# Kernel optimization log

Measured on AMD Instinct MI355X. Metric: run time of the kernel, lower is better.

## Reference

```python
import jax, jax.numpy as jnp
import numpy as np

B, G, A = 8, 32768, 64          # molecules, grid points/molecule, atomic orbitals/molecule
N_ORB, DIM, L_FUNC, N_OUT = 400, 128, 3, 1
EPS = 1e-12


def setup_inputs() -> dict:
    key = jax.random.key(0)
    ks = jax.random.split(key, 12)
    # interatomic/grid distances in Bohr-ish range (strictly positive)
    distance_matrices = jax.random.uniform(ks[0], (B, G, A), jnp.float32) * 10.0 + 0.05
    quantum_numbers = jax.random.randint(ks[1], (B, A), 0, 3, jnp.int32)   # q-1 in {0,1,2}
    atomic_orbitals = jax.random.randint(ks[2], (B, A), 0, N_ORB, jnp.int32)
    N_electrons = jax.random.uniform(ks[3], (B,), jnp.float32) * 50.0 + 10.0
    coef_table = jax.random.normal(ks[4], (N_ORB, DIM), jnp.float32) * 0.1
    zeta_table = jnp.ones((N_ORB, 1), jnp.float32)   # nn.init.ones_
    W_pre_w = jax.random.normal(ks[5], (DIM, 1), jnp.float32) * 0.1
    W_pre_b = jax.random.normal(ks[6], (DIM,), jnp.float32) * 0.01
    W_func_w = jax.random.normal(ks[7], (L_FUNC, DIM, DIM), jnp.float32) * (1.0 / np.sqrt(DIM))
    W_func_b = jax.random.normal(ks[8], (L_FUNC, DIM), jnp.float32) * 0.01
    W_prop_w = jax.random.normal(ks[9], (N_OUT, DIM), jnp.float32) * (1.0 / np.sqrt(DIM))
    W_prop_b = jax.random.normal(ks[10], (N_OUT,), jnp.float32) * 0.01
    return dict(distance_matrices=distance_matrices, quantum_numbers=quantum_numbers,
                atomic_orbitals=atomic_orbitals, N_electrons=N_electrons,
                coef_table=coef_table, zeta_table=zeta_table,
                W_pre_w=W_pre_w, W_pre_b=W_pre_b,
                W_func_w=W_func_w, W_func_b=W_func_b,
                W_prop_w=W_prop_w, W_prop_b=W_prop_b)


def reference(distance_matrices, quantum_numbers, atomic_orbitals, N_electrons,
              coef_table, zeta_table, W_pre_w, W_pre_b, W_func_w, W_func_b,
              W_prop_w, W_prop_b):
    d = distance_matrices                                   # [B,G,A]
    q = quantum_numbers.astype(jnp.float32) + 1.0           # principal quantum number {1,2,3}
    z = zeta_table[atomic_orbitals][..., 0]                 # [B,A] orbital exponents
    # GTO basis: d^(q-1) * exp(-(z*d)^2); block-diagonal padding (d=1e6 -> 0) is
    # equivalent to this batched per-molecule form.
    gto = d ** (q[:, None, :] - 1.0) * jnp.exp(-(z[:, None, :] * d) ** 2)
    gto = gto / jnp.maximum(jnp.sqrt(jnp.sum(gto * gto, 1, keepdims=True)), EPS)
    # per-molecule L2-normalized LCAO coefficients (F.normalize over AO axis)
    c = coef_table[atomic_orbitals]                         # [B,A,D]
    c = c / jnp.maximum(jnp.sqrt(jnp.sum(c * c, 1, keepdims=True)), EPS)
    # LCAO: molecular orbitals, then per-molecule normalization over grid points
    mo = jnp.einsum('bga,bad->bgd', gto, c)                 # [B,G,D]
    mo = mo / jnp.maximum(jnp.sqrt(jnp.sum(mo * mo, 1, keepdims=True)), EPS)
    mo = jnp.sqrt(N_electrons / DIM)[:, None, None] * mo
    densities = jnp.sum(mo * mo, -1, keepdims=True)         # [B,G,1]
    # DNN-based energy functional
    v = densities * W_pre_w[:, 0] + W_pre_b                 # [B,G,D]  (Linear(1,dim))
    for l in range(L_FUNC):
        v = jax.nn.relu(jnp.einsum('bgd,ed->bge', v, W_func_w[l]) + W_func_b[l])
    final = jnp.sum(v, 1)                                   # operation == 'sum' over grid
    E_xcH = final @ W_prop_w.T + W_prop_b                   # [B,N_OUT]
    return E_xcH
```

## Files before the change

kernel.cpp:

```cpp
#include <hip/hip_runtime.h>
#include <stdint.h>


#define BB 8
#define GG 32768
#define AA 64
#define DD 128
#define EPSF 1e-12f

#define WS_M    0u
#define WS_ZQ   131072u
#define WS_CN   135168u
#define WS_UW   397312u
#define WS_CCT  398336u
#define WS_W2   529408u
#define WS_W3   562176u

typedef __attribute__((ext_vector_type(8))) short bf16x8;
typedef __attribute__((ext_vector_type(4))) float f32x4;

__device__ __forceinline__ unsigned short f2bf(float f) {
    union { float f; unsigned int u; } x; x.f = f;
    unsigned int u = x.u + 0x7FFFu + ((x.u >> 16) & 1u);
    return (unsigned short)(u >> 16);
}
__device__ __forceinline__ float bfround(float f) {
    union { float f; unsigned int u; } x; x.f = f;
    unsigned int u = x.u + 0x7FFFu + ((x.u >> 16) & 1u);
    x.u = u & 0xFFFF0000u;
    return x.f;
}

__global__ __launch_bounds__(256)
void k_prep(const int* __restrict__ q, const int* __restrict__ ao,
            const float* __restrict__ coef, const float* __restrict__ zeta,
            const float* __restrict__ wpre_w, const float* __restrict__ wpre_b,
            const float* __restrict__ wfunc_w, const float* __restrict__ wfunc_b,
            const float* __restrict__ wprop_b, float* __restrict__ out,
            char* __restrict__ ws)
{
    int tid = blockIdx.x * 256 + threadIdx.x;
    if (tid < 32768) {
        int lsel = tid >> 14;
        int idx = tid & 16383;
        unsigned short* dst = (unsigned short*)(ws + (lsel == 0 ? WS_W2 : WS_W3));
        dst[idx] = f2bf(wfunc_w[(lsel + 1) * 16384 + idx]);
    } else if (tid < 33792) {
        int i = tid - 32768;
        int b = i >> 7, dd = i & 127;
        float s = 0.f;
        for (int a = 0; a < AA; ++a) {
            float v = coef[ao[b * AA + a] * DD + dd];
            s += v * v;
        }
        float inv = 1.f / fmaxf(sqrtf(s), EPSF);
        float* cn = (float*)(ws + WS_CN);
        for (int a = 0; a < AA; ++a)
            cn[((size_t)b * AA + a) * DD + dd] = coef[ao[b * AA + a] * DD + dd] * inv;
    } else if (tid < 34304) {
        int i = tid - 33792;
        int b = i >> 6, a = i & 63;
        float* zq = (float*)(ws + WS_ZQ);
        zq[(b * AA + a) * 2 + 0] = zeta[ao[b * AA + a]];
        zq[(b * AA + a) * 2 + 1] = (float)q[b * AA + a];
    } else if (tid < 34432) {
        int e = tid - 34304;
        float su = 0.f, sw = 0.f;
        for (int dd = 0; dd < DD; ++dd) {
            float wv = wfunc_w[e * DD + dd];
            su += wv * wpre_w[dd];
            sw += wv * wpre_b[dd];
        }
        float* uw = (float*)(ws + WS_UW);
        uw[e] = su;
        uw[128 + e] = sw + wfunc_b[e];
    } else if (tid < 34440) {
        out[tid - 34432] = wprop_b[0];
    } else if (tid < 67208) {
        ((float*)(ws + WS_M))[tid - 34440] = 0.f;
    }
}

__global__ __launch_bounds__(128)
void k_corr(const float* __restrict__ wfunc_w, const float* __restrict__ wfunc_b,
            const float* __restrict__ wprop_w, float* __restrict__ out,
            char* __restrict__ ws)
{
    __shared__ float v1e[128], v1b[128], v2e[128], v2b[128];
    __shared__ float part[2];
    int t = threadIdx.x;
    const float* uw = (const float*)(ws + WS_UW);
    float w0 = uw[128 + t];
    float r = fmaxf(w0, 0.f);
    v1e[t] = r;
    v1b[t] = bfround(r);
    __syncthreads();
    float ze = wfunc_b[128 + t], zb = ze;
    for (int dd = 0; dd < 128; ++dd) {
        float wv = wfunc_w[16384 + t * 128 + dd];
        ze += wv * v1e[dd];
        zb += bfround(wv) * v1b[dd];
    }
    v2e[t] = fmaxf(ze, 0.f);
    v2b[t] = bfround(fmaxf(zb, 0.f));
    __syncthreads();
    float ye = wfunc_b[256 + t], yb = ye;
    for (int dd = 0; dd < 128; ++dd) {
        float wv = wfunc_w[32768 + t * 128 + dd];
        ye += wv * v2e[dd];
        yb += bfround(wv) * v2b[dd];
    }
    float wpv = wprop_w[t];
    float diff = (fmaxf(ye, 0.f) - fmaxf(yb, 0.f)) * wpv;
    #pragma unroll
    for (int m = 1; m < 64; m <<= 1) diff += __shfl_xor(diff, m);
    if ((t & 63) == 0) part[t >> 6] = diff;
    __syncthreads();
    if (t == 0) {
        float corr = (part[0] + part[1]) * (float)GG;
        #pragma unroll
        for (int b = 0; b < BB; ++b) atomicAdd(&out[b], corr);
    }
}

__global__ __launch_bounds__(512, 4)
void k_M(const float* __restrict__ dmat, char* __restrict__ ws)
{
    __shared__ unsigned short gs[8192];
    const int b = blockIdx.y;
    const int chunk = blockIdx.x;
    const int t = threadIdx.x;
    const int g4 = t & 31;
    const int a4 = t >> 5;

    const float* zqp = (const float*)(ws + WS_ZQ) + b * 128;
    float4 zq0 = *(const float4*)(zqp + a4 * 8);
    float4 zq1 = *(const float4*)(zqp + a4 * 8 + 4);
    float zz[4] = {zq0.x, zq0.z, zq1.x, zq1.z};
    float qm[4] = {zq0.y, zq0.w, zq1.y, zq1.w};

    const int wv = t >> 6, l = t & 63;
    const int ta = wv >> 1, tb0 = (wv & 1) * 2;
    const int lrow = l & 15, lk = l >> 4;

    const float* dbase = dmat + (size_t)b * GG * AA + (size_t)chunk * 512 * AA;

    f32x4 acc[2];
    acc[0] = (f32x4){0.f, 0.f, 0.f, 0.f};
    acc[1] = (f32x4){0.f, 0.f, 0.f, 0.f};

    float4 pf[4];
    #pragma unroll
    for (int gg = 0; gg < 4; ++gg)
        pf[gg] = *(const float4*)(dbase + (size_t)(g4 * 4 + gg) * AA + a4 * 4);

    for (int tt = 0; tt < 4; ++tt) {
        float gv[4][4];
        #pragma unroll
        for (int gg = 0; gg < 4; ++gg) {
            float dvv[4] = {pf[gg].x, pf[gg].y, pf[gg].z, pf[gg].w};
            #pragma unroll
            for (int j = 0; j < 4; ++j) {
                float ttv = zz[j] * dvv[j];
                float ex = __expf(-ttv * ttv);
                float pw = (qm[j] < 0.5f) ? 1.f : ((qm[j] < 1.5f) ? dvv[j] : dvv[j] * dvv[j]);
                gv[gg][j] = pw * ex;
            }
        }
        if (tt < 3) {
            #pragma unroll
            for (int gg = 0; gg < 4; ++gg)
                pf[gg] = *(const float4*)(dbase + (size_t)((tt + 1) * 128 + g4 * 4 + gg) * AA + a4 * 4);
        }
        #pragma unroll
        for (int j = 0; j < 4; ++j) {
            int a = a4 * 4 + j;
            unsigned int lo = (unsigned int)f2bf(gv[0][j]) | ((unsigned int)f2bf(gv[1][j]) << 16);
            unsigned int hi = (unsigned int)f2bf(gv[2][j]) | ((unsigned int)f2bf(gv[3][j]) << 16);
            int off = a * 256 + ((g4 * 8) ^ ((a & 7) << 4));
            *(uint2*)((char*)gs + off) = make_uint2(lo, hi);
        }
        __syncthreads();
        #pragma unroll
        for (int kt = 0; kt < 4; ++kt) {
            int colB = kt * 64 + lk * 16;
            int ra = ta * 16 + lrow;
            bf16x8 af = *(const bf16x8*)((const char*)gs + ra * 256 + (colB ^ ((ra & 7) << 4)));
            #pragma unroll
            for (int jj = 0; jj < 2; ++jj) {
                int rb = (tb0 + jj) * 16 + lrow;
                bf16x8 bv = *(const bf16x8*)((const char*)gs + rb * 256 + (colB ^ ((rb & 7) << 4)));
                acc[jj] = __builtin_amdgcn_mfma_f32_16x16x32_bf16(af, bv, acc[jj], 0, 0, 0);
            }
        }
        __syncthreads();
    }
    float* Mg = (float*)(ws + WS_M) + b * 4096;
    #pragma unroll
    for (int jj = 0; jj < 2; ++jj)
        #pragma unroll
        for (int r = 0; r < 4; ++r)
            atomicAdd(&Mg[(ta * 16 + lk * 4 + r) * 64 + (tb0 + jj) * 16 + lrow], acc[jj][r]);
}

__global__ __launch_bounds__(256)
void k_cct(const float* __restrict__ Ne, char* __restrict__ ws)
{
    __shared__ float M[64][64];
    __shared__ float e_s[128][65];
    __shared__ float inv_na[64];
    __shared__ float alpha[128];
    const int b = blockIdx.x, t = threadIdx.x;
    const float* Mg = (const float*)(ws + WS_M) + b * 4096;
    for (int i = t; i < 4096; i += 256) ((float*)M)[i] = Mg[i];
    __syncthreads();
    if (t < 64) inv_na[t] = 1.f / fmaxf(sqrtf(M[t][t]), EPSF);
    __syncthreads();
    const float* cn = (const float*)(ws + WS_CN) + (size_t)b * AA * DD;
    for (int i = t; i < 8192; i += 256) {
        int a = i >> 7, dd = i & 127;
        e_s[dd][a] = cn[a * DD + dd] * inv_na[a];
    }
    __syncthreads();
    const int d = t >> 1, half = t & 1;
    float y[32];
    #pragma unroll
    for (int j = 0; j < 32; ++j) y[j] = 0.f;
    for (int a = 0; a < 64; ++a) {
        float ea = e_s[d][a];
        const float4* Mr = (const float4*)&M[a][half * 32];
        #pragma unroll 8
        for (int j4 = 0; j4 < 8; ++j4) {
            float4 mv = Mr[j4];
            y[4 * j4 + 0] += ea * mv.x; y[4 * j4 + 1] += ea * mv.y;
            y[4 * j4 + 2] += ea * mv.z; y[4 * j4 + 3] += ea * mv.w;
        }
    }
    float s = 0.f;
    #pragma unroll 8
    for (int j = 0; j < 32; ++j) s += e_s[d][half * 32 + j] * y[j];
    s += __shfl_xor(s, 1);
    if (half == 0) alpha[d] = sqrtf(Ne[b] * (1.f / 128.f)) / fmaxf(sqrtf(s), EPSF);
    __syncthreads();
    unsigned short* cct = (unsigned short*)(ws + WS_CCT) + (size_t)b * 8192;
    for (int i = t; i < 8192; i += 256) {
        int dd = i >> 6, a = i & 63;
        cct[i] = f2bf(e_s[dd][a] * alpha[dd]);
    }
}

__global__ __launch_bounds__(512, 4)
void k_main(const float* __restrict__ dmat, const float* __restrict__ wfunc_b,
            const float* __restrict__ wprop_w, float* __restrict__ out,
            char* __restrict__ ws)
{
    __shared__ char bufA[32768];
    __shared__ float dens[128];
    __shared__ float bsum;

    const int t = threadIdx.x;
    const int b = blockIdx.x >> 8;
    const int tile = blockIdx.x & 255;

    const int wv = t >> 6, l = t & 63;
    const int gsel = wv >> 1, dsel = wv & 1;
    const int lrow = l & 15, lk = l >> 4;
    const int srow = t >> 2, q4 = t & 3;

    const char* Wcct = (const char*)(ws + WS_CCT) + (size_t)b * 16384u;
    const char* W2g  = (const char*)(ws + WS_W2);
    const char* W3g  = (const char*)(ws + WS_W3);
    const float* zqp = (const float*)(ws + WS_ZQ) + b * 128;
    const float* uwp = (const float*)(ws + WS_UW);

    if (t < 128) dens[t] = 0.f;
    if (t == 0) bsum = 0.f;

    {
        const float* drow = dmat + ((size_t)b * GG + (size_t)tile * 128 + srow) * AA + q4 * 16;
        #pragma unroll
        for (int c = 0; c < 2; ++c) {
            float4 d0 = *(const float4*)(drow + c * 8);
            float4 d1 = *(const float4*)(drow + c * 8 + 4);
            const float* zb = zqp + (q4 * 16 + c * 8) * 2;
            float dvv[8] = {d0.x, d0.y, d0.z, d0.w, d1.x, d1.y, d1.z, d1.w};
            unsigned int wd[4];
            #pragma unroll
            for (int h = 0; h < 4; ++h) {
                unsigned short q2[2];
                #pragma unroll
                for (int jj = 0; jj < 2; ++jj) {
                    int j = h * 2 + jj;
                    float zzv = zb[j * 2], qmv = zb[j * 2 + 1];
                    float dv = dvv[j];
                    float ttv = zzv * dv;
                    float ex = __expf(-ttv * ttv);
                    float pw = (qmv < 0.5f) ? 1.f : ((qmv < 1.5f) ? dv : dv * dv);
                    q2[jj] = f2bf(pw * ex);
                }
                wd[h] = (unsigned int)q2[0] | ((unsigned int)q2[1] << 16);
            }
            int colB = q4 * 32 + c * 16;
            *(uint4*)(bufA + srow * 128 + (colB ^ ((srow & 7) << 4))) =
                make_uint4(wd[0], wd[1], wd[2], wd[3]);
        }
    }
    __syncthreads();

    {
        f32x4 acc[2][4];
        #pragma unroll
        for (int i = 0; i < 2; ++i)
            #pragma unroll
            for (int j = 0; j < 4; ++j) acc[i][j] = (f32x4){0.f, 0.f, 0.f, 0.f};
        #pragma unroll
        for (int kt = 0; kt < 2; ++kt) {
            int colB = kt * 64 + lk * 16;
            bf16x8 af[2], bv[4];
            #pragma unroll
            for (int i = 0; i < 2; ++i) {
                int gr = (gsel * 2 + i) * 16 + lrow;
                af[i] = *(const bf16x8*)(bufA + gr * 128 + (colB ^ ((gr & 7) << 4)));
            }
            #pragma unroll
            for (int j = 0; j < 4; ++j) {
                int dr = (dsel * 4 + j) * 16 + lrow;
                bv[j] = *(const bf16x8*)(Wcct + dr * 128 + colB);
            }
            #pragma unroll
            for (int i = 0; i < 2; ++i)
                #pragma unroll
                for (int j = 0; j < 4; ++j)
                    acc[i][j] = __builtin_amdgcn_mfma_f32_16x16x32_bf16(af[i], bv[j], acc[i][j], 0, 0, 0);
        }
        #pragma unroll
        for (int i = 0; i < 2; ++i) {
            float ds4[4] = {0.f, 0.f, 0.f, 0.f};
            #pragma unroll
            for (int j = 0; j < 4; ++j)
                #pragma unroll
                for (int r = 0; r < 4; ++r) { float m = acc[i][j][r]; ds4[r] += m * m; }
            #pragma unroll
            for (int r = 0; r < 4; ++r) {
                float vv = ds4[r];
                vv += __shfl_xor(vv, 1); vv += __shfl_xor(vv, 2);
                vv += __shfl_xor(vv, 4); vv += __shfl_xor(vv, 8);
                if (lrow == 0) atomicAdd(&dens[(gsel * 2 + i) * 16 + lk * 4 + r], vv);
            }
        }
    }
    __syncthreads();

    {
        float dv = dens[srow];
        #pragma unroll
        for (int c = 0; c < 4; ++c) {
            int di0 = q4 * 32 + c * 8;
            float4 ua = *(const float4*)(uwp + di0);
            float4 ub = *(const float4*)(uwp + di0 + 4);
            float4 wa = *(const float4*)(uwp + 128 + di0);
            float4 wb = *(const float4*)(uwp + 128 + di0 + 4);
            float uu[8] = {ua.x, ua.y, ua.z, ua.w, ub.x, ub.y, ub.z, ub.w};
            float wwv[8] = {wa.x, wa.y, wa.z, wa.w, wb.x, wb.y, wb.z, wb.w};
            unsigned int wd[4];
            #pragma unroll
            for (int h = 0; h < 4; ++h) {
                unsigned short q2[2];
                #pragma unroll
                for (int jj = 0; jj < 2; ++jj)
                    q2[jj] = f2bf(fmaxf(dv * uu[h * 2 + jj] + wwv[h * 2 + jj], 0.f));
                wd[h] = (unsigned int)q2[0] | ((unsigned int)q2[1] << 16);
            }
            int colB = q4 * 64 + c * 16;
            *(uint4*)(bufA + srow * 256 + (colB ^ ((srow & 7) << 4))) =
                make_uint4(wd[0], wd[1], wd[2], wd[3]);
        }
    }
    __syncthreads();

    f32x4 acc2[2][4];
    {
        #pragma unroll
        for (int i = 0; i < 2; ++i)
            #pragma unroll
            for (int j = 0; j < 4; ++j) acc2[i][j] = (f32x4){0.f, 0.f, 0.f, 0.f};
        #pragma unroll
        for (int kt = 0; kt < 4; ++kt) {
            int colB = kt * 64 + lk * 16;
            bf16x8 af[2], bv[4];
            #pragma unroll
            for (int i = 0; i < 2; ++i) {
                int gr = (gsel * 2 + i) * 16 + lrow;
                af[i] = *(const bf16x8*)(bufA + gr * 256 + (colB ^ ((gr & 7) << 4)));
            }
            #pragma unroll
            for (int j = 0; j < 4; ++j) {
                int er = (dsel * 4 + j) * 16 + lrow;
                bv[j] = *(const bf16x8*)(W2g + er * 256 + colB);
            }
            #pragma unroll
            for (int i = 0; i < 2; ++i)
                #pragma unroll
                for (int j = 0; j < 4; ++j)
                    acc2[i][j] = __builtin_amdgcn_mfma_f32_16x16x32_bf16(af[i], bv[j], acc2[i][j], 0, 0, 0);
        }
    }
    __syncthreads();

    #pragma unroll
    for (int j = 0; j < 4; ++j) {
        int e = (dsel * 4 + j) * 16 + lrow;
        float bias = wfunc_b[128 + e];
        #pragma unroll
        for (int i = 0; i < 2; ++i)
            #pragma unroll
            for (int r = 0; r < 4; ++r) {
                int g = (gsel * 2 + i) * 16 + lk * 4 + r;
                float vv = fmaxf(acc2[i][j][r] + bias, 0.f);
                *(unsigned short*)(bufA + g * 256 + ((e * 2) ^ ((g & 7) << 4))) = f2bf(vv);
            }
    }
    __syncthreads();

    f32x4 acc3[2][4];
    {
        #pragma unroll
        for (int i = 0; i < 2; ++i)
            #pragma unroll
            for (int j = 0; j < 4; ++j) acc3[i][j] = (f32x4){0.f, 0.f, 0.f, 0.f};
        #pragma unroll
        for (int kt = 0; kt < 4; ++kt) {
            int colB = kt * 64 + lk * 16;
            bf16x8 af[2], bv[4];
            #pragma unroll
            for (int i = 0; i < 2; ++i) {
                int gr = (gsel * 2 + i) * 16 + lrow;
                af[i] = *(const bf16x8*)(bufA + gr * 256 + (colB ^ ((gr & 7) << 4)));
            }
            #pragma unroll
            for (int j = 0; j < 4; ++j) {
                int er = (dsel * 4 + j) * 16 + lrow;
                bv[j] = *(const bf16x8*)(W3g + er * 256 + colB);
            }
            #pragma unroll
            for (int i = 0; i < 2; ++i)
                #pragma unroll
                for (int j = 0; j < 4; ++j)
                    acc3[i][j] = __builtin_amdgcn_mfma_f32_16x16x32_bf16(af[i], bv[j], acc3[i][j], 0, 0, 0);
        }
    }

    float esum = 0.f;
    #pragma unroll
    for (int j = 0; j < 4; ++j) {
        int e = (dsel * 4 + j) * 16 + lrow;
        float bias = wfunc_b[256 + e], wpv = wprop_w[e];
        #pragma unroll
        for (int i = 0; i < 2; ++i)
            #pragma unroll
            for (int r = 0; r < 4; ++r)
                esum += fmaxf(acc3[i][j][r] + bias, 0.f) * wpv;
    }
    #pragma unroll
    for (int m = 1; m < 64; m <<= 1) esum += __shfl_xor(esum, m);
    if (l == 0) atomicAdd(&bsum, esum);
    __syncthreads();
    if (t == 0) atomicAdd(&out[b], bsum);
}

extern "C" void kernel_launch(void* const* d_in, const int* in_sizes, int n_in,
                              void* d_out, int out_size, void* d_ws, size_t ws_size,
                              hipStream_t stream)
{
    const float* dmat    = (const float*)d_in[0];
    const int*   q       = (const int*)d_in[1];
    const int*   ao      = (const int*)d_in[2];
    const float* Ne      = (const float*)d_in[3];
    const float* coef    = (const float*)d_in[4];
    const float* zeta    = (const float*)d_in[5];
    const float* wpre_w  = (const float*)d_in[6];
    const float* wpre_b  = (const float*)d_in[7];
    const float* wfunc_w = (const float*)d_in[8];
    const float* wfunc_b = (const float*)d_in[9];
    const float* wprop_w = (const float*)d_in[10];
    const float* wprop_b = (const float*)d_in[11];
    float* out = (float*)d_out;
    char*  ws  = (char*)d_ws;

    k_prep<<<263, 256, 0, stream>>>(q, ao, coef, zeta, wpre_w, wpre_b,
                                    wfunc_w, wfunc_b, wprop_b, out, ws);
    k_corr<<<1, 128, 0, stream>>>(wfunc_w, wfunc_b, wprop_w, out, ws);
    k_M<<<dim3(64, 8), 512, 0, stream>>>(dmat, ws);
    k_cct<<<8, 256, 0, stream>>>(Ne, ws);
    k_main<<<2048, 512, 0, stream>>>(dmat, wfunc_b, wprop_w, out, ws);
}
```

Baseline: 278.3 us.

## Restructure k_main to per-wave tiles in registers and replicate k_M atomics

k_main now assigns each wave its own 16 grid rows. The GTO values go straight into MFMA A-fragments from registers, and densities are reduced with shuffles instead of through shared memory. Most LDS staging and block barriers between the three GEMM stages go away, and blocks shrink to 256 threads. k_M is reorganized around 256-point chunks with double-buffered LDS and wider swizzles. Its atomic accumulation is spread over 8 replica buffers plus a reduction kernel to cut atomic contention, at the cost of an extra memset and an extra launch.

Measured after the change: 321.3 us. 1.15x slower.

```diff
diff --git a/kernel.cpp b/kernel.cpp
--- a/kernel.cpp
+++ b/kernel.cpp
@@ -15,6 +15,7 @@
 #define WS_CCT  398336u
 #define WS_W2   529408u
 #define WS_W3   562176u
+#define WS_M8   594944u
 
 typedef __attribute__((ext_vector_type(8))) short bf16x8;
 typedef __attribute__((ext_vector_type(4))) float f32x4;
@@ -29,6 +30,12 @@
     unsigned int u = x.u + 0x7FFFu + ((x.u >> 16) & 1u);
     x.u = u & 0xFFFF0000u;
     return x.f;
+}
+__device__ __forceinline__ float gto_eval(float dv, float zz, float qm) {
+    float ttv = zz * dv;
+    float ex = __expf(-ttv * ttv);
+    float pw = (qm < 0.5f) ? 1.f : ((qm < 1.5f) ? dv : dv * dv);
+    return pw * ex;
 }
 
 __global__ __launch_bounds__(256)
@@ -61,8 +68,8 @@
         int i = tid - 33792;
         int b = i >> 6, a = i & 63;
         float* zq = (float*)(ws + WS_ZQ);
-        zq[(b * AA + a) * 2 + 0] = zeta[ao[b * AA + a]];
-        zq[(b * AA + a) * 2 + 1] = (float)q[b * AA + a];
+        zq[b * 128 + a]      = zeta[ao[b * AA + a]];
+        zq[b * 128 + 64 + a] = (float)q[b * AA + a];
     } else if (tid < 34432) {
         int e = tid - 34304;
         float su = 0.f, sw = 0.f;
@@ -123,84 +130,86 @@
     }
 }
 
-__global__ __launch_bounds__(512, 4)
+template<int NREP>
+__global__ __launch_bounds__(256, 4)
 void k_M(const float* __restrict__ dmat, char* __restrict__ ws)
 {
-    __shared__ unsigned short gs[8192];
+    __shared__ unsigned short gs[2][8192];
     const int b = blockIdx.y;
     const int chunk = blockIdx.x;
     const int t = threadIdx.x;
-    const int g4 = t & 31;
-    const int a4 = t >> 5;
-
-    const float* zqp = (const float*)(ws + WS_ZQ) + b * 128;
-    float4 zq0 = *(const float4*)(zqp + a4 * 8);
-    float4 zq1 = *(const float4*)(zqp + a4 * 8 + 4);
-    float zz[4] = {zq0.x, zq0.z, zq1.x, zq1.z};
-    float qm[4] = {zq0.y, zq0.w, zq1.y, zq1.w};
-
+    const int g4 = t & 31, a8 = t >> 5;
     const int wv = t >> 6, l = t & 63;
-    const int ta = wv >> 1, tb0 = (wv & 1) * 2;
     const int lrow = l & 15, lk = l >> 4;
 
-    const float* dbase = dmat + (size_t)b * GG * AA + (size_t)chunk * 512 * AA;
-
-    f32x4 acc[2];
-    acc[0] = (f32x4){0.f, 0.f, 0.f, 0.f};
-    acc[1] = (f32x4){0.f, 0.f, 0.f, 0.f};
-
-    float4 pf[4];
-    #pragma unroll
-    for (int gg = 0; gg < 4; ++gg)
-        pf[gg] = *(const float4*)(dbase + (size_t)(g4 * 4 + gg) * AA + a4 * 4);
-
-    for (int tt = 0; tt < 4; ++tt) {
-        float gv[4][4];
+    const float* zzp = (const float*)(ws + WS_ZQ) + b * 128;
+    float4 za = *(const float4*)(zzp + a8 * 8);
+    float4 zbv = *(const float4*)(zzp + a8 * 8 + 4);
+    float4 qa = *(const float4*)(zzp + 64 + a8 * 8);
+    float4 qb = *(const float4*)(zzp + 64 + a8 * 8 + 4);
+    float zz8[8] = {za.x, za.y, za.z, za.w, zbv.x, zbv.y, zbv.z, zbv.w};
+    float qm8[8] = {qa.x, qa.y, qa.z, qa.w, qb.x, qb.y, qb.z, qb.w};
+
+    const float* dbase = dmat + ((size_t)b * GG + (size_t)chunk * 256) * AA;
+
+    #pragma unroll
+    for (int tt = 0; tt < 2; ++tt) {
+        float gv[4][8];
         #pragma unroll
         for (int gg = 0; gg < 4; ++gg) {
-            float dvv[4] = {pf[gg].x, pf[gg].y, pf[gg].z, pf[gg].w};
+            const float* rp = dbase + (size_t)(tt * 128 + g4 * 4 + gg) * AA + a8 * 8;
+            float4 x0 = *(const float4*)rp;
+            float4 x1 = *(const float4*)(rp + 4);
+            float dv8[8] = {x0.x, x0.y, x0.z, x0.w, x1.x, x1.y, x1.z, x1.w};
             #pragma unroll
-            for (int j = 0; j < 4; ++j) {
-                float ttv = zz[j] * dvv[j];
-                float ex = __expf(-ttv * ttv);
-                float pw = (qm[j] < 0.5f) ? 1.f : ((qm[j] < 1.5f) ? dvv[j] : dvv[j] * dvv[j]);
-                gv[gg][j] = pw * ex;
-            }
-        }
-        if (tt < 3) {
-            #pragma unroll
-            for (int gg = 0; gg < 4; ++gg)
-                pf[gg] = *(const float4*)(dbase + (size_t)((tt + 1) * 128 + g4 * 4 + gg) * AA + a4 * 4);
-        }
-        #pragma unroll
-        for (int j = 0; j < 4; ++j) {
-            int a = a4 * 4 + j;
+            for (int j = 0; j < 8; ++j) gv[gg][j] = gto_eval(dv8[j], zz8[j], qm8[j]);
+        }
+        #pragma unroll
+        for (int j = 0; j < 8; ++j) {
+            int a = a8 * 8 + j;
             unsigned int lo = (unsigned int)f2bf(gv[0][j]) | ((unsigned int)f2bf(gv[1][j]) << 16);
             unsigned int hi = (unsigned int)f2bf(gv[2][j]) | ((unsigned int)f2bf(gv[3][j]) << 16);
-            int off = a * 256 + ((g4 * 8) ^ ((a & 7) << 4));
-            *(uint2*)((char*)gs + off) = make_uint2(lo, hi);
-        }
-        __syncthreads();
+            *(uint2*)((char*)gs[tt] + a * 256 + ((g4 * 8) ^ ((a & 15) << 4))) = make_uint2(lo, hi);
+        }
+    }
+    __syncthreads();
+
+    f32x4 acc[4];
+    #pragma unroll
+    for (int rb = 0; rb < 4; ++rb) acc[rb] = (f32x4){0.f, 0.f, 0.f, 0.f};
+    #pragma unroll
+    for (int tt = 0; tt < 2; ++tt)
         #pragma unroll
         for (int kt = 0; kt < 4; ++kt) {
             int colB = kt * 64 + lk * 16;
-            int ra = ta * 16 + lrow;
-            bf16x8 af = *(const bf16x8*)((const char*)gs + ra * 256 + (colB ^ ((ra & 7) << 4)));
+            int ra = wv * 16 + lrow;
+            bf16x8 af = *(const bf16x8*)((const char*)gs[tt] + ra * 256 + (colB ^ ((ra & 15) << 4)));
             #pragma unroll
-            for (int jj = 0; jj < 2; ++jj) {
-                int rb = (tb0 + jj) * 16 + lrow;
-                bf16x8 bv = *(const bf16x8*)((const char*)gs + rb * 256 + (colB ^ ((rb & 7) << 4)));
-                acc[jj] = __builtin_amdgcn_mfma_f32_16x16x32_bf16(af, bv, acc[jj], 0, 0, 0);
+            for (int rb = 0; rb < 4; ++rb) {
+                int rr = rb * 16 + lrow;
+                bf16x8 bv = *(const bf16x8*)((const char*)gs[tt] + rr * 256 + (colB ^ ((rr & 15) << 4)));
+                acc[rb] = __builtin_amdgcn_mfma_f32_16x16x32_bf16(af, bv, acc[rb], 0, 0, 0);
             }
         }
-        __syncthreads();
-    }
-    float* Mg = (float*)(ws + WS_M) + b * 4096;
-    #pragma unroll
-    for (int jj = 0; jj < 2; ++jj)
+
+    float* Mg = (float*)(ws + (NREP > 1 ? WS_M8 + (unsigned)(chunk & (NREP - 1)) * 131072u
+                                        : WS_M)) + b * 4096;
+    #pragma unroll
+    for (int rb = 0; rb < 4; ++rb)
         #pragma unroll
         for (int r = 0; r < 4; ++r)
-            atomicAdd(&Mg[(ta * 16 + lk * 4 + r) * 64 + (tb0 + jj) * 16 + lrow], acc[jj][r]);
+            atomicAdd(&Mg[(wv * 16 + lk * 4 + r) * 64 + rb * 16 + lrow], acc[rb][r]);
+}
+
+__global__ __launch_bounds__(256)
+void k_red(char* __restrict__ ws)
+{
+    int i = blockIdx.x * 256 + threadIdx.x;
+    const float* rp = (const float*)(ws + WS_M8);
+    float s = 0.f;
+    #pragma unroll
+    for (int r = 0; r < 8; ++r) s += rp[r * 32768 + i];
+    ((float*)(ws + WS_M))[i] = s;
 }
 
 __global__ __launch_bounds__(256)
@@ -249,220 +258,139 @@
     }
 }
 
-__global__ __launch_bounds__(512, 4)
+__global__ __launch_bounds__(256, 4)
 void k_main(const float* __restrict__ dmat, const float* __restrict__ wfunc_b,
             const float* __restrict__ wprop_w, float* __restrict__ out,
             char* __restrict__ ws)
 {
-    __shared__ char bufA[32768];
-    __shared__ float dens[128];
+    __shared__ char v2buf[16384];
     __shared__ float bsum;
 
     const int t = threadIdx.x;
-    const int b = blockIdx.x >> 8;
-    const int tile = blockIdx.x & 255;
-
+    const int b = blockIdx.x >> 9;
+    const int tile = blockIdx.x & 511;
     const int wv = t >> 6, l = t & 63;
-    const int gsel = wv >> 1, dsel = wv & 1;
     const int lrow = l & 15, lk = l >> 4;
-    const int srow = t >> 2, q4 = t & 3;
-
-    const char* Wcct = (const char*)(ws + WS_CCT) + (size_t)b * 16384u;
-    const char* W2g  = (const char*)(ws + WS_W2);
-    const char* W3g  = (const char*)(ws + WS_W3);
-    const float* zqp = (const float*)(ws + WS_ZQ) + b * 128;
+
+    if (t == 0) bsum = 0.f;
+
+    const char* Wcct = (const char*)ws + WS_CCT + (size_t)b * 16384u;
+    const char* W2g  = (const char*)ws + WS_W2;
+    const char* W3g  = (const char*)ws + WS_W3;
+    const float* zzp = (const float*)(ws + WS_ZQ) + b * 128;
     const float* uwp = (const float*)(ws + WS_UW);
 
-    if (t < 128) dens[t] = 0.f;
-    if (t == 0) bsum = 0.f;
-
+    const float* drow = dmat + ((size_t)b * GG + (size_t)tile * 64 + wv * 16 + lrow) * AA;
+
+    f32x4 acc[8];
+    #pragma unroll
+    for (int j = 0; j < 8; ++j) acc[j] = (f32x4){0.f, 0.f, 0.f, 0.f};
+    #pragma unroll
+    for (int kt = 0; kt < 2; ++kt) {
+        const int ab = kt * 32 + lk * 8;
+        float4 d0 = *(const float4*)(drow + ab);
+        float4 d1 = *(const float4*)(drow + ab + 4);
+        float4 z0 = *(const float4*)(zzp + ab);
+        float4 z1 = *(const float4*)(zzp + ab + 4);
+        float4 q0 = *(const float4*)(zzp + 64 + ab);
+        float4 q1 = *(const float4*)(zzp + 64 + ab + 4);
+        float dv8[8] = {d0.x, d0.y, d0.z, d0.w, d1.x, d1.y, d1.z, d1.w};
+        float zz8[8] = {z0.x, z0.y, z0.z, z0.w, z1.x, z1.y, z1.z, z1.w};
+        float qm8[8] = {q0.x, q0.y, q0.z, q0.w, q1.x, q1.y, q1.z, q1.w};
+        bf16x8 af;
+        #pragma unroll
+        for (int jj = 0; jj < 8; ++jj)
+            af[jj] = (short)f2bf(gto_eval(dv8[jj], zz8[jj], qm8[jj]));
+        #pragma unroll
+        for (int j = 0; j < 8; ++j) {
+            bf16x8 bv = *(const bf16x8*)(Wcct + (j * 16 + lrow) * 128 + kt * 64 + lk * 16);
+            acc[j] = __builtin_amdgcn_mfma_f32_16x16x32_bf16(af, bv, acc[j], 0, 0, 0);
+        }
+    }
+
+    float p0 = 0.f, p1 = 0.f, p2 = 0.f, p3 = 0.f;
+    #pragma unroll
+    for (int j = 0; j < 8; ++j) {
+        p0 += acc[j][0] * acc[j][0];
+        p1 += acc[j][1] * acc[j][1];
+        p2 += acc[j][2] * acc[j][2];
+        p3 += acc[j][3] * acc[j][3];
+    }
+    #pragma unroll
+    for (int m = 1; m < 16; m <<= 1) {
+        p0 += __shfl_xor(p0, m); p1 += __shfl_xor(p1, m);
+        p2 += __shfl_xor(p2, m); p3 += __shfl_xor(p3, m);
+    }
     {
-        const float* drow = dmat + ((size_t)b * GG + (size_t)tile * 128 + srow) * AA + q4 * 16;
-        #pragma unroll
-        for (int c = 0; c < 2; ++c) {
-            float4 d0 = *(const float4*)(drow + c * 8);
-            float4 d1 = *(const float4*)(drow + c * 8 + 4);
-            const float* zb = zqp + (q4 * 16 + c * 8) * 2;
-            float dvv[8] = {d0.x, d0.y, d0.z, d0.w, d1.x, d1.y, d1.z, d1.w};
-            unsigned int wd[4];
-            #pragma unroll
-            for (int h = 0; h < 4; ++h) {
-                unsigned short q2[2];
-                #pragma unroll
-                for (int jj = 0; jj < 2; ++jj) {
-                    int j = h * 2 + jj;
-                    float zzv = zb[j * 2], qmv = zb[j * 2 + 1];
-                    float dv = dvv[j];
-                    float ttv = zzv * dv;
-                    float ex = __expf(-ttv * ttv);
-                    float pw = (qmv < 0.5f) ? 1.f : ((qmv < 1.5f) ? dv : dv * dv);
-                    q2[jj] = f2bf(pw * ex);
-                }
-                wd[h] = (unsigned int)q2[0] | ((unsigned int)q2[1] << 16);
-            }
-            int colB = q4 * 32 + c * 16;
-            *(uint4*)(bufA + srow * 128 + (colB ^ ((srow & 7) << 4))) =
-                make_uint4(wd[0], wd[1], wd[2], wd[3]);
-        }
-    }
-    __syncthreads();
-
-    {
-        f32x4 acc[2][4];
-        #pragma unroll
-        for (int i = 0; i < 2; ++i)
-            #pragma unroll
-            for (int j = 0; j < 4; ++j) acc[i][j] = (f32x4){0.f, 0.f, 0.f, 0.f};
-        #pragma unroll
-        for (int kt = 0; kt < 2; ++kt) {
-            int colB = kt * 64 + lk * 16;
-            bf16x8 af[2], bv[4];
-            #pragma unroll
-            for (int i = 0; i < 2; ++i) {
-                int gr = (gsel * 2 + i) * 16 + lrow;
-                af[i] = *(const bf16x8*)(bufA + gr * 128 + (colB ^ ((gr & 7) << 4)));
-            }
-            #pragma unroll
-            for (int j = 0; j < 4; ++j) {
-                int dr = (dsel * 4 + j) * 16 + lrow;
-                bv[j] = *(const bf16x8*)(Wcct + dr * 128 + colB);
-            }
-            #pragma unroll
-            for (int i = 0; i < 2; ++i)
-                #pragma unroll
-                for (int j = 0; j < 4; ++j)
-                    acc[i][j] = __builtin_amdgcn_mfma_f32_16x16x32_bf16(af[i], bv[j], acc[i][j], 0, 0, 0);
-        }
-        #pragma unroll
-        for (int i = 0; i < 2; ++i) {
-            float ds4[4] = {0.f, 0.f, 0.f, 0.f};
-            #pragma unroll
-            for (int j = 0; j < 4; ++j)
-                #pragma unroll
-                for (int r = 0; r < 4; ++r) { float m = acc[i][j][r]; ds4[r] += m * m; }
-            #pragma unroll
-            for (int r = 0; r < 4; ++r) {
-                float vv = ds4[r];
-                vv += __shfl_xor(vv, 1); vv += __shfl_xor(vv, 2);
-                vv += __shfl_xor(vv, 4); vv += __shfl_xor(vv, 8);
-                if (lrow == 0) atomicAdd(&dens[(gsel * 2 + i) * 16 + lk * 4 + r], vv);
-            }
-        }
-    }
-    __syncthreads();
-
-    {
-        float dv = dens[srow];
-        #pragma unroll
-        for (int c = 0; c < 4; ++c) {
-            int di0 = q4 * 32 + c * 8;
-            float4 ua = *(const float4*)(uwp + di0);
-            float4 ub = *(const float4*)(uwp + di0 + 4);
-            float4 wa = *(const float4*)(uwp + 128 + di0);
-            float4 wb = *(const float4*)(uwp + 128 + di0 + 4);
-            float uu[8] = {ua.x, ua.y, ua.z, ua.w, ub.x, ub.y, ub.z, ub.w};
-            float wwv[8] = {wa.x, wa.y, wa.z, wa.w, wb.x, wb.y, wb.z, wb.w};
-            unsigned int wd[4];
-            #pragma unroll
-            for (int h = 0; h < 4; ++h) {
-                unsigned short q2[2];
-                #pragma unroll
-                for (int jj = 0; jj < 2; ++jj)
-                    q2[jj] = f2bf(fmaxf(dv * uu[h * 2 + jj] + wwv[h * 2 + jj], 0.f));
-                wd[h] = (unsigned int)q2[0] | ((unsigned int)q2[1] << 16);
-            }
-            int colB = q4 * 64 + c * 16;
-            *(uint4*)(bufA + srow * 256 + (colB ^ ((srow & 7) << 4))) =
-                make_uint4(wd[0], wd[1], wd[2], wd[3]);
-        }
-    }
-    __syncthreads();
-
-    f32x4 acc2[2][4];
-    {
-        #pragma unroll
-        for (int i = 0; i < 2; ++i)
-            #pragma unroll
-            for (int j = 0; j < 4; ++j) acc2[i][j] = (f32x4){0.f, 0.f, 0.f, 0.f};
-        #pragma unroll
-        for (int kt = 0; kt < 4; ++kt) {
-            int colB = kt * 64 + lk * 16;
-            bf16x8 af[2], bv[4];
-            #pragma unroll
-            for (int i = 0; i < 2; ++i) {
-                int gr = (gsel * 2 + i) * 16 + lrow;
-                af[i] = *(const bf16x8*)(bufA + gr * 256 + (colB ^ ((gr & 7) << 4)));
-            }
-            #pragma unroll
-            for (int j = 0; j < 4; ++j) {
-                int er = (dsel * 4 + j) * 16 + lrow;
-                bv[j] = *(const bf16x8*)(W2g + er * 256 + colB);
-            }
-            #pragma unroll
-            for (int i = 0; i < 2; ++i)
-                #pragma unroll
-                for (int j = 0; j < 4; ++j)
-                    acc2[i][j] = __builtin_amdgcn_mfma_f32_16x16x32_bf16(af[i], bv[j], acc2[i][j], 0, 0, 0);
-        }
-    }
-    __syncthreads();
-
-    #pragma unroll
-    for (int j = 0; j < 4; ++j) {
-        int e = (dsel * 4 + j) * 16 + lrow;
-        float bias = wfunc_b[128 + e];
-        #pragma unroll
-        for (int i = 0; i < 2; ++i)
-            #pragma unroll
-            for (int r = 0; r < 4; ++r) {
-                int g = (gsel * 2 + i) * 16 + lk * 4 + r;
-                float vv = fmaxf(acc2[i][j][r] + bias, 0.f);
-                *(unsigned short*)(bufA + g * 256 + ((e * 2) ^ ((g & 7) << 4))) = f2bf(vv);
-            }
-    }
-    __syncthreads();
-
-    f32x4 acc3[2][4];
-    {
-        #pragma unroll
-        for (int i = 0; i < 2; ++i)
-            #pragma unroll
-            for (int j = 0; j < 4; ++j) acc3[i][j] = (f32x4){0.f, 0.f, 0.f, 0.f};
-        #pragma unroll
-        for (int kt = 0; kt < 4; ++kt) {
-            int colB = kt * 64 + lk * 16;
-            bf16x8 af[2], bv[4];
-            #pragma unroll
-            for (int i = 0; i < 2; ++i) {
-                int gr = (gsel * 2 + i) * 16 + lrow;
-                af[i] = *(const bf16x8*)(bufA + gr * 256 + (colB ^ ((gr & 7) << 4)));
-            }
-            #pragma unroll
-            for (int j = 0; j < 4; ++j) {
-                int er = (dsel * 4 + j) * 16 + lrow;
-                bv[j] = *(const bf16x8*)(W3g + er * 256 + colB);
-            }
-            #pragma unroll
-            for (int i = 0; i < 2; ++i)
-                #pragma unroll
-                for (int j = 0; j < 4; ++j)
-                    acc3[i][j] = __builtin_amdgcn_mfma_f32_16x16x32_bf16(af[i], bv[j], acc3[i][j], 0, 0, 0);
+        int src = (lrow >> 2) << 4;
+        float e0 = __shfl(p0, src), e1 = __shfl(p1, src);
+        float e2 = __shfl(p2, src), e3 = __shfl(p3, src);
+        int rr = lrow & 3;
+        p0 = (rr == 0) ? e0 : (rr == 1) ? e1 : (rr == 2) ? e2 : e3;
+    }
+    const float dv = p0;
+
+    f32x4 acc2[8];
+    #pragma unroll
+    for (int j = 0; j < 8; ++j) acc2[j] = (f32x4){0.f, 0.f, 0.f, 0.f};
+    #pragma unroll
+    for (int kt = 0; kt < 4; ++kt) {
+        const int db = kt * 32 + lk * 8;
+        float4 u0 = *(const float4*)(uwp + db);
+        float4 u1 = *(const float4*)(uwp + db + 4);
+        float4 w0 = *(const float4*)(uwp + 128 + db);
+        float4 w1 = *(const float4*)(uwp + 128 + db + 4);
+        float uu[8] = {u0.x, u0.y, u0.z, u0.w, u1.x, u1.y, u1.z, u1.w};
+        float ww[8] = {w0.x, w0.y, w0.z, w0.w, w1.x, w1.y, w1.z, w1.w};
+        bf16x8 af;
+        #pragma unroll
+        for (int jj = 0; jj < 8; ++jj)
+            af[jj] = (short)f2bf(fmaxf(dv * uu[jj] + ww[jj], 0.f));
+        #pragma unroll
+        for (int j = 0; j < 8; ++j) {
+            bf16x8 bv = *(const bf16x8*)(W2g + (j * 16 + lrow) * 256 + kt * 64 + lk * 16);
+            acc2[j] = __builtin_amdgcn_mfma_f32_16x16x32_bf16(af, bv, acc2[j], 0, 0, 0);
+        }
+    }
+
+    char* vb = v2buf + wv * 4096;
+    #pragma unroll
+    for (int j = 0; j < 8; ++j) {
+        float bias = wfunc_b[128 + j * 16 + lrow];
+        #pragma unroll
+        for (int r = 0; r < 4; ++r) {
+            int row = lk * 4 + r;
+            int colb = (j * 32 + lrow * 2) ^ ((row & 15) << 4);
+            *(unsigned short*)(vb + row * 256 + colb) = f2bf(fmaxf(acc2[j][r] + bias, 0.f));
+        }
+    }
+
+    f32x4 acc3[8];
+    #pragma unroll
+    for (int j = 0; j < 8; ++j) acc3[j] = (f32x4){0.f, 0.f, 0.f, 0.f};
+    #pragma unroll
+    for (int kt = 0; kt < 4; ++kt) {
+        bf16x8 af = *(const bf16x8*)(vb + lrow * 256 +
+                                     ((kt * 64 + lk * 16) ^ ((lrow & 15) << 4)));
+        #pragma unroll
+        for (int j = 0; j < 8; ++j) {
+            bf16x8 bv = *(const bf16x8*)(W3g + (j * 16 + lrow) * 256 + kt * 64 + lk * 16);
+            acc3[j] = __builtin_amdgcn_mfma_f32_16x16x32_bf16(af, bv, acc3[j], 0, 0, 0);
         }
     }
 
     float esum = 0.f;
     #pragma unroll
-    for (int j = 0; j < 4; ++j) {
-        int e = (dsel * 4 + j) * 16 + lrow;
-        float bias = wfunc_b[256 + e], wpv = wprop_w[e];
-        #pragma unroll
-        for (int i = 0; i < 2; ++i)
-            #pragma unroll
-            for (int r = 0; r < 4; ++r)
-                esum += fmaxf(acc3[i][j][r] + bias, 0.f) * wpv;
+    for (int j = 0; j < 8; ++j) {
+        float bias = wfunc_b[256 + j * 16 + lrow];
+        float wpv = wprop_w[j * 16 + lrow];
+        #pragma unroll
+        for (int r = 0; r < 4; ++r)
+            esum += fmaxf(acc3[j][r] + bias, 0.f) * wpv;
     }
     #pragma unroll
     for (int m = 1; m < 64; m <<= 1) esum += __shfl_xor(esum, m);
+    __syncthreads();
     if (l == 0) atomicAdd(&bsum, esum);
     __syncthreads();
     if (t == 0) atomicAdd(&out[b], bsum);
@@ -487,10 +415,18 @@
     float* out = (float*)d_out;
     char*  ws  = (char*)d_ws;
 
+    const bool rep = ws_size >= (size_t)(WS_M8 + 1048576u);
+
     k_prep<<<263, 256, 0, stream>>>(q, ao, coef, zeta, wpre_w, wpre_b,
                                     wfunc_w, wfunc_b, wprop_b, out, ws);
     k_corr<<<1, 128, 0, stream>>>(wfunc_w, wfunc_b, wprop_w, out, ws);
-    k_M<<<dim3(64, 8), 512, 0, stream>>>(dmat, ws);
-    k_cct<<<8, 256, 0, stream>>>(Ne, ws);
-    k_main<<<2048, 512, 0, stream>>>(dmat, wfunc_b, wprop_w, out, ws);
-}
+    if (rep) {
+        hipMemsetAsync(ws + WS_M8, 0, 1048576, stream);
+        k_M<8><<<dim3(128, BB), 256, 0, stream>>>(dmat, ws);
+        k_red<<<128, 256, 0, stream>>>(ws);
+    } else {
+        k_M<1><<<dim3(128, BB), 256, 0, stream>>>(dmat, ws);
+    }
+    k_cct<<<BB, 256, 0, stream>>>(Ne, ws);
+    k_main<<<4096, 256, 0, stream>>>(dmat, wfunc_b, wprop_w, out, ws);
+}
```
